# Performance work log

Measured on AMD Instinct MI355X. Metric: run time of the kernel, lower is better.

The kernel has to match this reference:

```python
import jax, jax.numpy as jnp
import numpy as np

B, T, C = 4, 1024, 1024
H, HKV, D = 16, 4, 64
GATE_CH = 12
ROPE_THETA = 10000.0


def _rms_norm(x):
    # F.rms_norm with default eps = machine epsilon of dtype, no learnable scale
    eps = jnp.finfo(x.dtype).eps
    ms = jnp.mean(jnp.square(x), axis=-1, keepdims=True)
    return x * jax.lax.rsqrt(ms + eps)


def _apply_rotary(x, cos, sin):
    # x: (B, T, h, D); cos/sin: (1, T, 1, D//2). Half-split rotation.
    d = x.shape[-1] // 2
    x1, x2 = x[..., :d], x[..., d:]
    y1 = x1 * cos + x2 * sin
    y2 = -x1 * sin + x2 * cos
    return jnp.concatenate([y1, y2], axis=-1)


def setup_inputs() -> dict:
    key = jax.random.key(0)
    ks = jax.random.split(key, 8)
    x = jax.random.normal(ks[0], (B, T, C), dtype=jnp.float32)
    ve = jax.random.normal(ks[1], (B, T, HKV * D), dtype=jnp.float32)
    # real RoPE tables, shape (1, T, 1, D//2)
    half = D // 2
    inv_freq = 1.0 / (ROPE_THETA ** (np.arange(half, dtype=np.float32) / half))
    freqs = np.arange(T, dtype=np.float32)[:, None] * inv_freq[None, :]
    cos = jnp.asarray(np.cos(freqs), dtype=jnp.float32).reshape(1, T, 1, half)
    sin = jnp.asarray(np.sin(freqs), dtype=jnp.float32).reshape(1, T, 1, half)
    s = 0.02
    Wq = jax.random.normal(ks[2], (H * D, C), dtype=jnp.float32) * s
    Wk = jax.random.normal(ks[3], (HKV * D, C), dtype=jnp.float32) * s
    Wv = jax.random.normal(ks[4], (HKV * D, C), dtype=jnp.float32) * s
    Wo = jax.random.normal(ks[5], (C, C), dtype=jnp.float32) * s
    Wg = jax.random.normal(ks[6], (HKV, GATE_CH), dtype=jnp.float32) * s
    return {"x": x, "ve": ve, "cos": cos, "sin": sin,
            "Wq": Wq, "Wk": Wk, "Wv": Wv, "Wo": Wo, "Wg": Wg,
            "window_size": 256}


def reference(x, ve, cos, sin, Wq, Wk, Wv, Wo, Wg, window_size):
    b, t, c = x.shape
    d = 2 * cos.shape[-1]
    h = Wq.shape[0] // d
    hkv = Wk.shape[0] // d
    rep = h // hkv

    q = (x @ Wq.T).reshape(b, t, h, d)
    k = (x @ Wk.T).reshape(b, t, hkv, d)
    v = (x @ Wv.T).reshape(b, t, hkv, d)

    # value-embedding sigmoid gate (3 * sigmoid of first 12 channels of x)
    gate = 3.0 * jax.nn.sigmoid(x[..., : Wg.shape[1]] @ Wg.T)  # (b, t, hkv)
    v = v + gate[..., None] * ve.reshape(b, t, hkv, d)

    q = _apply_rotary(q, cos, sin)
    k = _apply_rotary(k, cos, sin)
    q = _rms_norm(q) * 1.2
    k = _rms_norm(k) * 1.2

    # GQA attention with sliding-window causal mask (left=window_size, right=0)
    qg = q.reshape(b, t, hkv, rep, d)
    scale = 1.0 / jnp.sqrt(jnp.asarray(d, dtype=q.dtype))
    scores = jnp.einsum('bqgrd,bkgd->bgrqk', qg, k) * scale
    i = jnp.arange(t)[:, None]
    j = jnp.arange(t)[None, :]
    mask = (j <= i) & ((i - j) <= window_size)  # (t, t)
    scores = jnp.where(mask[None, None, None], scores, -jnp.inf)
    probs = jax.nn.softmax(scores, axis=-1)
    y = jnp.einsum('bgrqk,bkgd->bqgrd', probs, v).reshape(b, t, h * d)
    return y @ Wo.T
```

## Files before the change

kernel.cpp:

```cpp
#include <hip/hip_runtime.h>

typedef __bf16 v8bf __attribute__((ext_vector_type(8)));
typedef float v4f __attribute__((ext_vector_type(4)));
typedef unsigned int v4u __attribute__((ext_vector_type(4)));
typedef unsigned int v2u __attribute__((ext_vector_type(2)));
typedef unsigned short u16;

#define DEVI static __device__ __forceinline__

DEVI float bf2f(u16 u) {
    union { float f; unsigned int i; } c; c.i = ((unsigned int)u) << 16; return c.f;
}
DEVI u16 f2bf(float f) {
    union { __bf16 b; u16 u; } c; c.b = (__bf16)f;
    return c.u;
}

union Frag { v4u u; v8bf v; u16 h[8]; };

#define GLD16(gptr, lptr) __builtin_amdgcn_global_load_lds( \
    (const __attribute__((address_space(1))) void*)(gptr),  \
    (__attribute__((address_space(3))) void*)(lptr), 16, 0, 0)

__global__ __launch_bounds__(256) void convert5(
    const float* __restrict__ x, const float* __restrict__ wq,
    const float* __restrict__ wk, const float* __restrict__ wv,
    const float* __restrict__ wo, u16* __restrict__ xb,
    u16* __restrict__ wb, u16* __restrict__ wob)
{
    const float* src; u16* dst; int n;
    switch (blockIdx.y) {
        case 0: src = x;  dst = xb;               n = 4096 * 1024; break;
        case 1: src = wq; dst = wb;               n = 1024 * 1024; break;
        case 2: src = wk; dst = wb + 1024 * 1024; n = 256 * 1024;  break;
        case 3: src = wv; dst = wb + 1280 * 1024; n = 256 * 1024;  break;
        default: src = wo; dst = wob;             n = 1024 * 1024; break;
    }
    const int stride = gridDim.x * 256 * 4;
    for (int i = (blockIdx.x * 256 + threadIdx.x) * 4; i < n; i += stride) {
        const float4 f = *(const float4*)(src + i);
        v2u p;
        p[0] = (unsigned int)f2bf(f.x) | ((unsigned int)f2bf(f.y) << 16);
        p[1] = (unsigned int)f2bf(f.z) | ((unsigned int)f2bf(f.w) << 16);
        *(v2u*)(dst + i) = p;
    }
}

template <bool F32OUT>
__global__ __launch_bounds__(256) void gemm_bt(
    const u16* __restrict__ A, const u16* __restrict__ B,
    void* __restrict__ Cv, int N)
{
    __shared__ __align__(16) u16 As[64 * 64];
    __shared__ __align__(16) u16 Bs[128 * 64];
    const int tid  = threadIdx.x;
    const int lane = tid & 63, l15 = lane & 15, quad = (lane >> 4) & 3;
    const int w    = tid >> 6;
    const int wr   = (w >> 1) * 32, wc = (w & 1) * 64;
    const int m0   = blockIdx.x * 64, n0 = blockIdx.y * 128;

    const u16* ab = A + m0 * 1024;
    const u16* bb = B + n0 * 1024;
    const int r0 = tid >> 3;
    const int c0 = (tid & 7) * 8;
    const u16* ag = ab + r0 * 1024 + c0;
    const u16* bg = bb + r0 * 1024 + c0;
    u16* al = &As[r0 * 64 + c0];
    u16* bl = &Bs[r0 * 64 + c0];

    v4f acc[2][4];
    const v4f vzero = {0.f, 0.f, 0.f, 0.f};
#pragma unroll
    for (int i = 0; i < 2; i++)
#pragma unroll
        for (int j = 0; j < 4; j++) acc[i][j] = vzero;

    for (int k0 = 0; k0 < 1024; k0 += 64) {
        __syncthreads();
        GLD16(ag + k0,             al);
        GLD16(ag + k0 + 32 * 1024, al + 32 * 64);
        GLD16(bg + k0,             bl);
        GLD16(bg + k0 + 32 * 1024, bl + 32 * 64);
        GLD16(bg + k0 + 64 * 1024, bl + 64 * 64);
        GLD16(bg + k0 + 96 * 1024, bl + 96 * 64);
        __syncthreads();
#pragma unroll
        for (int ks = 0; ks < 2; ks++) {
            v8bf af[2];
#pragma unroll
            for (int mi = 0; mi < 2; mi++)
                af[mi] = *(const v8bf*)&As[(wr + mi * 16 + l15) * 64 + ks * 32 + quad * 8];
#pragma unroll
            for (int ni = 0; ni < 4; ni++) {
                v8bf bv = *(const v8bf*)&Bs[(wc + ni * 16 + l15) * 64 + ks * 32 + quad * 8];
#pragma unroll
                for (int mi = 0; mi < 2; mi++)
                    acc[mi][ni] = __builtin_amdgcn_mfma_f32_16x16x32_bf16(af[mi], bv, acc[mi][ni], 0, 0, 0);
            }
        }
    }
#pragma unroll
    for (int mi = 0; mi < 2; mi++) {
        const int row = m0 + wr + mi * 16 + quad * 4;
#pragma unroll
        for (int ni = 0; ni < 4; ni++) {
            const int col = n0 + wc + ni * 16 + l15;
#pragma unroll
            for (int r = 0; r < 4; r++) {
                if (F32OUT) ((float*)Cv)[(row + r) * N + col] = acc[mi][ni][r];
                else        ((u16*)Cv)[(row + r) * N + col] = f2bf(acc[mi][ni][r]);
            }
        }
    }
}

__global__ __launch_bounds__(256) void fixup(
    const u16* __restrict__ qkv, const float* __restrict__ x,
    const float* __restrict__ ve, const float* __restrict__ cs,
    const float* __restrict__ sn, const float* __restrict__ Wg,
    u16* __restrict__ qn, u16* __restrict__ kn, u16* __restrict__ vn)
{
    const int token = blockIdx.x;
    const int pos   = token & 1023;
    const int tid   = threadIdx.x;
    const int hw    = tid >> 5, l = tid & 31;
    const float c = cs[pos * 32 + l];
    const float s = sn[pos * 32 + l];
#pragma unroll
    for (int it = 0; it < 3; it++) {
        const int task = it * 8 + hw;
        if (task < 20) {
            const u16* src; u16* dst;
            if (task < 16) { src = qkv + token * 1536 + task * 64;               dst = qn + token * 1024 + task * 64; }
            else           { src = qkv + token * 1536 + 1024 + (task - 16) * 64; dst = kn + token * 256 + (task - 16) * 64; }
            const float x1 = bf2f(src[l]), x2 = bf2f(src[32 + l]);
            const float y1 = x1 * c + x2 * s;
            const float y2 = x2 * c - x1 * s;
            float ss = y1 * y1 + y2 * y2;
#pragma unroll
            for (int off = 16; off >= 1; off >>= 1) ss += __shfl_xor(ss, off, 64);
            const float inv = rsqrtf(ss * (1.0f / 64.0f) + 1.1920929e-7f) * 1.2f;
            dst[l]      = f2bf(y1 * inv);
            dst[32 + l] = f2bf(y2 * inv);
        } else {
            const int g = task - 20;
            float dot = 0.f;
#pragma unroll
            for (int cc = 0; cc < 12; cc++)
                dot += x[token * 1024 + cc] * Wg[g * 12 + cc];
            const float gate = 3.f / (1.f + __expf(-dot));
            const u16*   vsrc  = qkv + token * 1536 + 1280 + g * 64;
            const float* vesrc = ve + token * 256 + g * 64;
            u16* vdst = vn + token * 256 + g * 64;
            vdst[l]      = f2bf(bf2f(vsrc[l])      + gate * vesrc[l]);
            vdst[32 + l] = f2bf(bf2f(vsrc[32 + l]) + gate * vesrc[32 + l]);
        }
    }
}

__global__ __launch_bounds__(256) void vtrans(
    const u16* __restrict__ vn, u16* __restrict__ vt)
{
    __shared__ __align__(16) u16 T[64 * 72];
    const int tid = threadIdx.x;
    const int t0  = blockIdx.x * 64, g = blockIdx.y, b = blockIdx.z;
    {
        const int row = tid >> 2, ch = (tid & 3) * 16;
        const int goff = (b * 1024 + t0 + row) * 256 + g * 64 + ch;
        *(v4u*)&T[row * 72 + ch]     = *(const v4u*)&vn[goff];
        *(v4u*)&T[row * 72 + ch + 8] = *(const v4u*)&vn[goff + 8];
    }
    __syncthreads();
    {
        const int d = tid >> 2, tc = (tid & 3) * 16;
        Frag o0, o1;
#pragma unroll
        for (int j = 0; j < 8; j++) {
            o0.h[j] = T[(tc + j) * 72 + d];
            o1.h[j] = T[(tc + 8 + j) * 72 + d];
        }
        u16* dst = vt + ((b * 4 + g) * 64 + d) * 1024 + t0 + tc;
        *(v4u*)dst       = o0.u;
        *(v4u*)(dst + 8) = o1.u;
    }
}

__global__ __launch_bounds__(256) void attn(
    const u16* __restrict__ qn, const u16* __restrict__ kn,
    const u16* __restrict__ vt, u16* __restrict__ yo)
{
    __shared__ __align__(16) u16 Ks[64 * 72];
    __shared__ __align__(16) u16 VTs[64 * 72];
    __shared__ __align__(16) u16 Ps[4][32 * 72];
    const int tid  = threadIdx.x;
    const int w    = tid >> 6, lane = tid & 63, l15 = lane & 15, quad = (lane >> 4) & 3;
    const int qb   = blockIdx.x, h = blockIdx.y, b = blockIdx.z;
    const int g    = h >> 2;
    const int qbase = qb * 128;
    const int qabs0 = qbase + w * 32;
    const int tok0  = b * 1024 + qabs0;
    u16* pw = Ps[w];

    v8bf qf[2][2];
#pragma unroll
    for (int mi = 0; mi < 2; mi++)
#pragma unroll
        for (int ks = 0; ks < 2; ks++) {
            Frag f;
            f.u = *(const v4u*)&qn[(tok0 + mi * 16 + l15) * 1024 + h * 64 + ks * 32 + quad * 8];
#pragma unroll
            for (int j = 0; j < 8; j++) f.h[j] = f2bf(0.125f * bf2f(f.h[j]));
            qf[mi][ks] = f.v;
        }

    v4f o[2][4];
    float li[2][4];
    const v4f vzero = {0.f, 0.f, 0.f, 0.f};
#pragma unroll
    for (int mi = 0; mi < 2; mi++) {
#pragma unroll
        for (int nd = 0; nd < 4; nd++) o[mi][nd] = vzero;
#pragma unroll
        for (int r = 0; r < 4; r++) li[mi][r] = 0.f;
    }

    const int kstart = (qbase >= 256) ? qbase - 256 : 0;
    const int kend   = qbase + 64;
    for (int kbase = kstart; kbase <= kend; kbase += 64) {
        __syncthreads();
        {
            const int row = tid >> 2, ch = (tid & 3) * 16;
            const int goff = (b * 1024 + kbase + row) * 256 + g * 64 + ch;
            *(v4u*)&Ks[row * 72 + ch]     = *(const v4u*)&kn[goff];
            *(v4u*)&Ks[row * 72 + ch + 8] = *(const v4u*)&kn[goff + 8];
            const u16* vsrc = vt + ((b * 4 + g) * 64 + row) * 1024 + kbase + ch;
            *(v4u*)&VTs[row * 72 + ch]     = *(const v4u*)vsrc;
            *(v4u*)&VTs[row * 72 + ch + 8] = *(const v4u*)(vsrc + 8);
        }
        __syncthreads();

        bool skip2[2][4], full2[2][4];
#pragma unroll
        for (int mi = 0; mi < 2; mi++)
#pragma unroll
            for (int ni = 0; ni < 4; ni++) {
                const int qw = qabs0 + mi * 16;
                const int left = kbase + ni * 16;
                skip2[mi][ni] = (left > qw + 15) || (qw - (left + 15) > 256);
                full2[mi][ni] = ((left + 15) <= qw) && ((qw + 15 - left) <= 256);
            }

#pragma unroll
        for (int mi = 0; mi < 2; mi++) {
#pragma unroll
            for (int ni = 0; ni < 4; ni++) {
                if (skip2[mi][ni]) {
#pragma unroll
                    for (int r = 0; r < 4; r++)
                        pw[(mi * 16 + quad * 4 + r) * 72 + ni * 16 + l15] = 0;
                    continue;
                }
                v8bf kf0 = *(const v8bf*)&Ks[(ni * 16 + l15) * 72 + quad * 8];
                v8bf kf1 = *(const v8bf*)&Ks[(ni * 16 + l15) * 72 + 32 + quad * 8];
                v4f a = vzero;
                a = __builtin_amdgcn_mfma_f32_16x16x32_bf16(qf[mi][0], kf0, a, 0, 0, 0);
                a = __builtin_amdgcn_mfma_f32_16x16x32_bf16(qf[mi][1], kf1, a, 0, 0, 0);
                if (!full2[mi][ni]) {
                    const int kj = kbase + ni * 16 + l15;
#pragma unroll
                    for (int r = 0; r < 4; r++) {
                        const int qi = qabs0 + mi * 16 + quad * 4 + r;
                        if (!((kj <= qi) && (qi - kj <= 256))) a[r] = -1e30f;
                    }
                }
#pragma unroll
                for (int r = 0; r < 4; r++) {
                    const float p = __expf(a[r] - 12.0f);
                    li[mi][r] += p;
                    pw[(mi * 16 + quad * 4 + r) * 72 + ni * 16 + l15] = f2bf(p);
                }
            }
        }

#pragma unroll
        for (int mi = 0; mi < 2; mi++)
#pragma unroll
            for (int ks = 0; ks < 2; ks++) {
                if (skip2[mi][2 * ks] && skip2[mi][2 * ks + 1]) continue;
                v8bf af = *(const v8bf*)&pw[(mi * 16 + l15) * 72 + ks * 32 + quad * 8];
#pragma unroll
                for (int nd = 0; nd < 4; nd++) {
                    v8bf bv = *(const v8bf*)&VTs[(nd * 16 + l15) * 72 + ks * 32 + quad * 8];
                    o[mi][nd] = __builtin_amdgcn_mfma_f32_16x16x32_bf16(af, bv, o[mi][nd], 0, 0, 0);
                }
            }
    }

#pragma unroll
    for (int mi = 0; mi < 2; mi++) {
#pragma unroll
        for (int off = 8; off >= 1; off >>= 1)
#pragma unroll
            for (int r = 0; r < 4; r++)
                li[mi][r] += __shfl_xor(li[mi][r], off, 64);
        float inv[4];
#pragma unroll
        for (int r = 0; r < 4; r++) inv[r] = 1.f / li[mi][r];
#pragma unroll
        for (int nd = 0; nd < 4; nd++) {
            const int col = h * 64 + nd * 16 + l15;
#pragma unroll
            for (int r = 0; r < 4; r++) {
                const int row = tok0 + mi * 16 + quad * 4 + r;
                yo[row * 1024 + col] = f2bf(o[mi][nd][r] * inv[r]);
            }
        }
    }
}

extern "C" void kernel_launch(void* const* d_in, const int* in_sizes, int n_in,
                              void* d_out, int out_size, void* d_ws, size_t ws_size,
                              hipStream_t stream)
{
    const float* x  = (const float*)d_in[0];
    const float* ve = (const float*)d_in[1];
    const float* cs = (const float*)d_in[2];
    const float* sn = (const float*)d_in[3];
    const float* Wq = (const float*)d_in[4];
    const float* Wk = (const float*)d_in[5];
    const float* Wv = (const float*)d_in[6];
    const float* Wo = (const float*)d_in[7];
    const float* Wg = (const float*)d_in[8];

    u16* xb  = (u16*)d_ws;
    u16* wb  = xb  + 4096 * 1024;
    u16* wob = wb  + 1536 * 1024;
    u16* qkv = wob + 1024 * 1024;
    u16* qn  = qkv + 4096 * 1536;
    u16* kn  = qn  + 4096 * 1024;
    u16* vn  = kn  + 4096 * 256;
    u16* vt  = vn  + 4096 * 256;
    u16* ay  = qkv;

    convert5<<<dim3(512, 5), 256, 0, stream>>>(x, Wq, Wk, Wv, Wo, xb, wb, wob);
    gemm_bt<false><<<dim3(64, 12), 256, 0, stream>>>(xb, wb, (void*)qkv, 1536);
    fixup<<<4096, 256, 0, stream>>>(qkv, x, ve, cs, sn, Wg, qn, kn, vn);
    vtrans<<<dim3(16, 4, 4), 256, 0, stream>>>(vn, vt);
    attn<<<dim3(8, 16, 4), 256, 0, stream>>>(qn, kn, vt, ay);
    gemm_bt<true><<<dim3(64, 8), 256, 0, stream>>>(ay, wob, d_out, 1024);
}
```

Before: 168.0 us.

## Fuse RoPE, RMS norm and value gate into QKV GEMM epilogue

```diff
diff --git a/kernel.cpp b/kernel.cpp
--- a/kernel.cpp
+++ b/kernel.cpp
@@ -22,12 +22,25 @@
     (const __attribute__((address_space(1))) void*)(gptr),  \
     (__attribute__((address_space(3))) void*)(lptr), 16, 0, 0)
 
-__global__ __launch_bounds__(256) void convert5(
+__global__ __launch_bounds__(256) void convert6(
     const float* __restrict__ x, const float* __restrict__ wq,
     const float* __restrict__ wk, const float* __restrict__ wv,
-    const float* __restrict__ wo, u16* __restrict__ xb,
-    u16* __restrict__ wb, u16* __restrict__ wob)
-{
+    const float* __restrict__ wo, const float* __restrict__ Wg,
+    u16* __restrict__ xb, u16* __restrict__ wb, u16* __restrict__ wob,
+    float* __restrict__ gates)
+{
+    if (blockIdx.y == 5) {
+        const int stride = gridDim.x * 256;
+        for (int i = blockIdx.x * 256 + threadIdx.x; i < 4096 * 4; i += stride) {
+            const int token = i >> 2, g = i & 3;
+            float dot = 0.f;
+#pragma unroll
+            for (int c = 0; c < 12; c++)
+                dot += x[token * 1024 + c] * Wg[g * 12 + c];
+            gates[i] = 3.f / (1.f + __expf(-dot));
+        }
+        return;
+    }
     const float* src; u16* dst; int n;
     switch (blockIdx.y) {
         case 0: src = x;  dst = xb;               n = 4096 * 1024; break;
@@ -46,10 +59,13 @@
     }
 }
 
-template <bool F32OUT>
+template <bool QKV>
 __global__ __launch_bounds__(256) void gemm_bt(
     const u16* __restrict__ A, const u16* __restrict__ B,
-    void* __restrict__ Cv, int N)
+    void* __restrict__ Cv, int N,
+    const float* __restrict__ cs, const float* __restrict__ sn,
+    const float* __restrict__ gates, const float* __restrict__ ve,
+    u16* __restrict__ qn, u16* __restrict__ kn, u16* __restrict__ vn)
 {
     __shared__ __align__(16) u16 As[64 * 64];
     __shared__ __align__(16) u16 Bs[128 * 64];
@@ -99,61 +115,65 @@
             }
         }
     }
-#pragma unroll
-    for (int mi = 0; mi < 2; mi++) {
-        const int row = m0 + wr + mi * 16 + quad * 4;
-#pragma unroll
-        for (int ni = 0; ni < 4; ni++) {
-            const int col = n0 + wc + ni * 16 + l15;
+
+    if (!QKV) {
+#pragma unroll
+        for (int mi = 0; mi < 2; mi++) {
+            const int row = m0 + wr + mi * 16 + quad * 4;
+#pragma unroll
+            for (int ni = 0; ni < 4; ni++) {
+                const int col = n0 + wc + ni * 16 + l15;
+#pragma unroll
+                for (int r = 0; r < 4; r++)
+                    ((float*)Cv)[(row + r) * N + col] = acc[mi][ni][r];
+            }
+        }
+        return;
+    }
+
+    const int hcol = n0 + wc;
+    if (hcol < 1280) {
+        const bool isQ = (hcol < 1024);
+        u16* dst = isQ ? (qn + (hcol >> 6) * 64) : (kn + ((hcol - 1024) >> 6) * 64);
+        const int dstride = isQ ? 1024 : 256;
+#pragma unroll
+        for (int mi = 0; mi < 2; mi++) {
 #pragma unroll
             for (int r = 0; r < 4; r++) {
-                if (F32OUT) ((float*)Cv)[(row + r) * N + col] = acc[mi][ni][r];
-                else        ((u16*)Cv)[(row + r) * N + col] = f2bf(acc[mi][ni][r]);
-            }
-        }
-    }
-}
-
-__global__ __launch_bounds__(256) void fixup(
-    const u16* __restrict__ qkv, const float* __restrict__ x,
-    const float* __restrict__ ve, const float* __restrict__ cs,
-    const float* __restrict__ sn, const float* __restrict__ Wg,
-    u16* __restrict__ qn, u16* __restrict__ kn, u16* __restrict__ vn)
-{
-    const int token = blockIdx.x;
-    const int pos   = token & 1023;
-    const int tid   = threadIdx.x;
-    const int hw    = tid >> 5, l = tid & 31;
-    const float c = cs[pos * 32 + l];
-    const float s = sn[pos * 32 + l];
-#pragma unroll
-    for (int it = 0; it < 3; it++) {
-        const int task = it * 8 + hw;
-        if (task < 20) {
-            const u16* src; u16* dst;
-            if (task < 16) { src = qkv + token * 1536 + task * 64;               dst = qn + token * 1024 + task * 64; }
-            else           { src = qkv + token * 1536 + 1024 + (task - 16) * 64; dst = kn + token * 256 + (task - 16) * 64; }
-            const float x1 = bf2f(src[l]), x2 = bf2f(src[32 + l]);
-            const float y1 = x1 * c + x2 * s;
-            const float y2 = x2 * c - x1 * s;
-            float ss = y1 * y1 + y2 * y2;
-#pragma unroll
-            for (int off = 16; off >= 1; off >>= 1) ss += __shfl_xor(ss, off, 64);
-            const float inv = rsqrtf(ss * (1.0f / 64.0f) + 1.1920929e-7f) * 1.2f;
-            dst[l]      = f2bf(y1 * inv);
-            dst[32 + l] = f2bf(y2 * inv);
-        } else {
-            const int g = task - 20;
-            float dot = 0.f;
-#pragma unroll
-            for (int cc = 0; cc < 12; cc++)
-                dot += x[token * 1024 + cc] * Wg[g * 12 + cc];
-            const float gate = 3.f / (1.f + __expf(-dot));
-            const u16*   vsrc  = qkv + token * 1536 + 1280 + g * 64;
-            const float* vesrc = ve + token * 256 + g * 64;
-            u16* vdst = vn + token * 256 + g * 64;
-            vdst[l]      = f2bf(bf2f(vsrc[l])      + gate * vesrc[l]);
-            vdst[32 + l] = f2bf(bf2f(vsrc[32 + l]) + gate * vesrc[32 + l]);
+                const int row = m0 + wr + mi * 16 + quad * 4 + r;
+                const int pos = row & 1023;
+                const float c0 = cs[pos * 32 + l15],      s0 = sn[pos * 32 + l15];
+                const float c1 = cs[pos * 32 + 16 + l15], s1 = sn[pos * 32 + 16 + l15];
+                const float y0 = acc[mi][0][r] * c0 + acc[mi][2][r] * s0;
+                const float y2 = acc[mi][2][r] * c0 - acc[mi][0][r] * s0;
+                const float y1 = acc[mi][1][r] * c1 + acc[mi][3][r] * s1;
+                const float y3 = acc[mi][3][r] * c1 - acc[mi][1][r] * s1;
+                float ss = y0 * y0 + y1 * y1 + y2 * y2 + y3 * y3;
+#pragma unroll
+                for (int off = 8; off >= 1; off >>= 1)
+                    ss += __shfl_xor(ss, off, 64);
+                const float inv = rsqrtf(ss * (1.0f / 64.0f) + 1.1920929e-7f) * 1.2f;
+                u16* d = dst + row * dstride;
+                d[l15]      = f2bf(y0 * inv);
+                d[16 + l15] = f2bf(y1 * inv);
+                d[32 + l15] = f2bf(y2 * inv);
+                d[48 + l15] = f2bf(y3 * inv);
+            }
+        }
+    } else {
+        const int g = (hcol - 1280) >> 6;
+#pragma unroll
+        for (int mi = 0; mi < 2; mi++) {
+#pragma unroll
+            for (int r = 0; r < 4; r++) {
+                const int row = m0 + wr + mi * 16 + quad * 4 + r;
+                const float gate = gates[row * 4 + g];
+                u16* d = vn + row * 256 + g * 64;
+                const float* vesrc = ve + row * 256 + g * 64;
+#pragma unroll
+                for (int ni = 0; ni < 4; ni++)
+                    d[ni * 16 + l15] = f2bf(acc[mi][ni][r] + gate * vesrc[ni * 16 + l15]);
+            }
         }
     }
 }
@@ -209,7 +229,7 @@
             Frag f;
             f.u = *(const v4u*)&qn[(tok0 + mi * 16 + l15) * 1024 + h * 64 + ks * 32 + quad * 8];
 #pragma unroll
-            for (int j = 0; j < 8; j++) f.h[j] = f2bf(0.125f * bf2f(f.h[j]));
+            for (int j = 0; j < 8; j++) f.h[j] = f2bf(0.18033688f * bf2f(f.h[j]));
             qf[mi][ks] = f.v;
         }
 
@@ -275,7 +295,7 @@
                 }
 #pragma unroll
                 for (int r = 0; r < 4; r++) {
-                    const float p = __expf(a[r] - 12.0f);
+                    const float p = exp2f(a[r] - 17.312340f);
                     li[mi][r] += p;
                     pw[(mi * 16 + quad * 4 + r) * 72 + ni * 16 + l15] = f2bf(p);
                 }
@@ -332,20 +352,22 @@
     const float* Wo = (const float*)d_in[7];
     const float* Wg = (const float*)d_in[8];
 
-    u16* xb  = (u16*)d_ws;
-    u16* wb  = xb  + 4096 * 1024;
-    u16* wob = wb  + 1536 * 1024;
-    u16* qkv = wob + 1024 * 1024;
-    u16* qn  = qkv + 4096 * 1536;
-    u16* kn  = qn  + 4096 * 1024;
-    u16* vn  = kn  + 4096 * 256;
-    u16* vt  = vn  + 4096 * 256;
-    u16* ay  = qkv;
-
-    convert5<<<dim3(512, 5), 256, 0, stream>>>(x, Wq, Wk, Wv, Wo, xb, wb, wob);
-    gemm_bt<false><<<dim3(64, 12), 256, 0, stream>>>(xb, wb, (void*)qkv, 1536);
-    fixup<<<4096, 256, 0, stream>>>(qkv, x, ve, cs, sn, Wg, qn, kn, vn);
+    u16*   xb    = (u16*)d_ws;
+    u16*   wb    = xb  + 4096 * 1024;
+    u16*   wob   = wb  + 1536 * 1024;
+    u16*   qn    = wob + 1024 * 1024;
+    u16*   kn    = qn  + 4096 * 1024;
+    u16*   vn    = kn  + 4096 * 256;
+    u16*   vt    = vn  + 4096 * 256;
+    u16*   ay    = vt  + 4096 * 256;
+    float* gates = (float*)(ay + 4096 * 1024);
+
+    convert6<<<dim3(512, 6), 256, 0, stream>>>(x, Wq, Wk, Wv, Wo, Wg, xb, wb, wob, gates);
+    gemm_bt<true><<<dim3(64, 12), 256, 0, stream>>>(xb, wb, nullptr, 1536,
+                                                    cs, sn, gates, ve, qn, kn, vn);
     vtrans<<<dim3(16, 4, 4), 256, 0, stream>>>(vn, vt);
     attn<<<dim3(8, 16, 4), 256, 0, stream>>>(qn, kn, vt, ay);
-    gemm_bt<true><<<dim3(64, 8), 256, 0, stream>>>(ay, wob, d_out, 1024);
-}
+    gemm_bt<false><<<dim3(64, 8), 256, 0, stream>>>(ay, wob, d_out, 1024,
+                                                    nullptr, nullptr, nullptr, nullptr,
+                                                    nullptr, nullptr, nullptr);
+}
```

Result: faster. 160.7 us (-4.4%).
